# Kernel optimization log

Measured on AMD Instinct MI355X. Metric: run time of the kernel, lower is better.

Reference implementation:

```python
import jax, jax.numpy as jnp
import numpy as np

N = 10000          # nodes
E = 160000         # edges (before self-loops)
F_IN = 256
H, C = 8, 64       # heads, channels per head
NUM_CLASSES = 40
NEG_SLOPE = 0.2    # PyG GATConv default leaky_relu slope


def setup_inputs() -> dict:
    key = jax.random.key(0)
    ks = jax.random.split(key, 16)
    s = 0.1  # keep logits tame
    x = jax.random.normal(ks[0], (N, F_IN), jnp.float32)
    edge_index = jax.random.randint(ks[1], (2, E), 0, N)
    W0 = jax.random.normal(ks[2], (F_IN, H * C), jnp.float32) / np.sqrt(F_IN)
    a_src0 = jax.random.normal(ks[3], (H, C), jnp.float32) * s
    a_dst0 = jax.random.normal(ks[4], (H, C), jnp.float32) * s
    b0 = jnp.zeros((H * C,), jnp.float32)
    W1 = jax.random.normal(ks[5], (H * C, H * C), jnp.float32) / np.sqrt(H * C)
    a_src1 = jax.random.normal(ks[6], (H, C), jnp.float32) * s
    a_dst1 = jax.random.normal(ks[7], (H, C), jnp.float32) * s
    b1 = jnp.zeros((H * C,), jnp.float32)
    W2 = jax.random.normal(ks[8], (H * C, NUM_CLASSES), jnp.float32) / np.sqrt(H * C)
    a_src2 = jax.random.normal(ks[9], (1, NUM_CLASSES), jnp.float32) * s
    a_dst2 = jax.random.normal(ks[10], (1, NUM_CLASSES), jnp.float32) * s
    b2 = jnp.zeros((NUM_CLASSES,), jnp.float32)
    return dict(x=x, edge_index=edge_index, W0=W0, a_src0=a_src0, a_dst0=a_dst0, b0=b0,
                W1=W1, a_src1=a_src1, a_dst1=a_dst1, b1=b1,
                W2=W2, a_src2=a_src2, a_dst2=a_dst2, b2=b2)


def gat_conv(x, src, dst, W, a_src, a_dst, b, concat):
    """PyG GATConv (eval mode: dropout = identity)."""
    n = x.shape[0]
    h, c = a_src.shape
    hx = (x @ W).reshape(n, h, c)                       # [N,H,C]
    al_s = jnp.sum(hx * a_src, axis=-1)                 # [N,H]
    al_d = jnp.sum(hx * a_dst, axis=-1)                 # [N,H]
    e = jax.nn.leaky_relu(al_s[src] + al_d[dst], NEG_SLOPE)  # [E,H]
    # neighbor softmax over incoming edges of each dst node
    m = jax.ops.segment_max(e, dst, num_segments=n)     # [N,H]
    ex = jnp.exp(e - m[dst])
    denom = jax.ops.segment_sum(ex, dst, num_segments=n)
    alpha = ex / (denom[dst] + 1e-16)                   # [E,H]
    msg = hx[src] * alpha[:, :, None]                   # [E,H,C]
    out = jax.ops.segment_sum(msg, dst, num_segments=n) # [N,H,C]
    out = out.reshape(n, h * c) if concat else out.mean(axis=1)
    return out + b


def reference(x, edge_index, W0, a_src0, a_dst0, b0, W1, a_src1, a_dst1, b1,
              W2, a_src2, a_dst2, b2):
    # add self-loops once (PyG GATConv add_self_loops=True)
    loops = jnp.arange(N, dtype=edge_index.dtype)
    src = jnp.concatenate([edge_index[0], loops])
    dst = jnp.concatenate([edge_index[1], loops])
    x = jax.nn.elu(gat_conv(x, src, dst, W0, a_src0, a_dst0, b0, True))
    x = jax.nn.elu(gat_conv(x, src, dst, W1, a_src1, a_dst1, b1, True))
    return gat_conv(x, src, dst, W2, a_src2, a_dst2, b2, False)
```

## Files before the change

### kernel.cpp

```cpp
#include <hip/hip_runtime.h>
#include <math.h>

#define NN 10000
#define EE 160000
#define ET 170000
#define FIN 256
#define HH 8
#define CC 64
#define HC 512
#define NCLS 40
#define ELLW 96

typedef unsigned short u16;
typedef unsigned int u32;
typedef _Float16 f16;
using f16x8 = __attribute__((ext_vector_type(8))) _Float16;
using f32x4 = __attribute__((ext_vector_type(4))) float;

#define MFMA16(a, b, c) __builtin_amdgcn_mfma_f32_16x16x32_f16((a), (b), (c), 0, 0, 0)

__global__ __launch_bounds__(256) void zero_int(int* p, int n) {
    int i = blockIdx.x * 256 + threadIdx.x;
    if (i < n) p[i] = 0;
}

__global__ __launch_bounds__(256) void scatter_ell(const int* __restrict__ ei,
                                                   int* __restrict__ cnt,
                                                   int* __restrict__ ell) {
    int e = blockIdx.x * 256 + threadIdx.x;
    if (e >= ET) return;
    int s, d;
    if (e < EE) { s = ei[e]; d = ei[EE + e]; }
    else        { s = e - EE; d = s; }
    int pos = atomicAdd(&cnt[d], 1);
    if (pos < ELLW) ell[(size_t)d * ELLW + pos] = s;
}

__global__ __launch_bounds__(256) void convW_kernel(const float* __restrict__ W0,
                                                    const float* __restrict__ W1,
                                                    const float* __restrict__ W2,
                                                    f16* __restrict__ w0T,
                                                    f16* __restrict__ w1T,
                                                    f16* __restrict__ w2T) {
    int i = blockIdx.x * 256 + threadIdx.x;
    if (i < HC * FIN) {
        int n = i >> 8, k = i & 255;
        w0T[i] = (f16)W0[(size_t)k * HC + n];
    } else if (i < HC * FIN + HC * HC) {
        int j = i - HC * FIN;
        int n = j >> 9, k = j & 511;
        w1T[j] = (f16)W1[(size_t)k * HC + n];
    } else if (i < HC * FIN + HC * HC + NCLS * HC) {
        int j = i - HC * FIN - HC * HC;
        int n = j >> 9, k = j & 511;
        w2T[j] = (f16)W2[(size_t)k * NCLS + n];
    }
}

template <int K, bool AF32>
__global__ __launch_bounds__(512) void gemm_attn(const void* __restrict__ Aptr,
                                                 const f16* __restrict__ BT,
                                                 const float* __restrict__ a_src,
                                                 const float* __restrict__ a_dst,
                                                 f16* __restrict__ hx2,
                                                 float* __restrict__ al_s,
                                                 float* __restrict__ al_d) {
    constexpr int KK = K / 32;
    constexpr int CH = K / 8;
    __shared__ f16 Bs[64 * K];
    int t = threadIdx.x;
    int hp = blockIdx.x;
    int lane = t & 63, w = t >> 6;
    int fm = lane & 15, g = lane >> 4;
    int bm = blockIdx.y * 128 + w * 16;
    int row = bm + fm;
    bool rok = row < NN;

    f16x8 af[KK];
    if (AF32) {
        const float* A = (const float*)Aptr;
#pragma unroll
        for (int kk = 0; kk < KK; ++kk) {
            float4 lo = make_float4(0.f, 0.f, 0.f, 0.f), hi = lo;
            if (rok) {
                const float* ap = A + (size_t)row * K + kk * 32 + g * 8;
                lo = *(const float4*)ap;
                hi = *(const float4*)(ap + 4);
            }
            f16x8 v;
            v[0] = (f16)lo.x; v[1] = (f16)lo.y; v[2] = (f16)lo.z; v[3] = (f16)lo.w;
            v[4] = (f16)hi.x; v[5] = (f16)hi.y; v[6] = (f16)hi.z; v[7] = (f16)hi.w;
            af[kk] = v;
        }
    } else {
        const f16* A = (const f16*)Aptr;
#pragma unroll
        for (int kk = 0; kk < KK; ++kk) {
            uint4 r = rok ? *(const uint4*)(A + (size_t)row * K + kk * 32 + g * 8)
                          : make_uint4(0u, 0u, 0u, 0u);
            af[kk] = __builtin_bit_cast(f16x8, r);
        }
    }

    for (int sl = 0; sl < 2; ++sl) {
        int h = hp * 2 + sl;
        const f16* bsrc = BT + (size_t)h * 64 * K;
        for (int c = t; c < 64 * CH; c += 512) {
            int brow = c / CH;
            int j = c - brow * CH;
            uint4 v = *(const uint4*)(bsrc + (size_t)brow * K + j * 8);
            *(uint4*)&Bs[(size_t)brow * K + ((j ^ (brow & 7)) * 8)] = v;
        }
        __syncthreads();

        f32x4 acc[4] = {};
#pragma unroll
        for (int kk = 0; kk < KK; ++kk) {
#pragma unroll
            for (int nt = 0; nt < 4; ++nt) {
                f16x8 b = *(const f16x8*)
                    &Bs[(nt * 16 + fm) * K + (((kk * 4 + g) ^ (fm & 7)) * 8)];
                acc[nt] = MFMA16(af[kk], b, acc[nt]);
            }
        }

        float asc[4], adc[4];
#pragma unroll
        for (int nt = 0; nt < 4; ++nt) {
            asc[nt] = a_src[h * 64 + nt * 16 + fm];
            adc[nt] = a_dst[h * 64 + nt * 16 + fm];
        }
#pragma unroll
        for (int r = 0; r < 4; ++r) {
            int orow = bm + g * 4 + r;
            float s = acc[0][r] * asc[0] + acc[1][r] * asc[1] +
                      acc[2][r] * asc[2] + acc[3][r] * asc[3];
            float d = acc[0][r] * adc[0] + acc[1][r] * adc[1] +
                      acc[2][r] * adc[2] + acc[3][r] * adc[3];
#pragma unroll
            for (int off = 1; off < 16; off <<= 1) {
                s += __shfl_xor(s, off);
                d += __shfl_xor(d, off);
            }
            if (orow < NN) {
                if (fm == 0) {
                    al_s[orow * 8 + h] = s;
                    al_d[orow * 8 + h] = d;
                }
#pragma unroll
                for (int nt = 0; nt < 4; ++nt)
                    hx2[(size_t)orow * HC + h * 64 + nt * 16 + fm] =
                        (f16)acc[nt][r];
            }
        }
        __syncthreads();
    }
}

__global__ __launch_bounds__(256) void gemm2_attn(const f16* __restrict__ A,
                                                  const f16* __restrict__ BT,
                                                  const float* __restrict__ a_src2,
                                                  const float* __restrict__ a_dst2,
                                                  float* __restrict__ hx40,
                                                  float* __restrict__ als2,
                                                  float* __restrict__ ald2) {
    __shared__ f16 Bs[48 * HC];
    int t = threadIdx.x;
    int lane = t & 63, w = t >> 6;
    int fm = lane & 15, g = lane >> 4;
    int bm = blockIdx.x * 64 + w * 16;
    int row = bm + fm;
    bool rok = row < NN;

    for (int c = t; c < 48 * 64; c += 256) {
        int brow = c >> 6, j = c & 63;
        uint4 v = make_uint4(0u, 0u, 0u, 0u);
        if (brow < NCLS) v = *(const uint4*)(BT + (size_t)brow * HC + j * 8);
        *(uint4*)&Bs[brow * HC + ((j ^ (brow & 7)) * 8)] = v;
    }

    f16x8 af[16];
#pragma unroll
    for (int kk = 0; kk < 16; ++kk) {
        uint4 r = rok ? *(const uint4*)(A + (size_t)row * HC + kk * 32 + g * 8)
                      : make_uint4(0u, 0u, 0u, 0u);
        af[kk] = __builtin_bit_cast(f16x8, r);
    }
    __syncthreads();

    f32x4 acc[3] = {};
#pragma unroll
    for (int kk = 0; kk < 16; ++kk) {
#pragma unroll
        for (int nt = 0; nt < 3; ++nt) {
            f16x8 b = *(const f16x8*)
                &Bs[(nt * 16 + fm) * HC + (((kk * 4 + g) ^ (fm & 7)) * 8)];
            acc[nt] = MFMA16(af[kk], b, acc[nt]);
        }
    }

    float a2s[3], a2d[3];
#pragma unroll
    for (int nt = 0; nt < 3; ++nt) {
        int col = nt * 16 + fm;
        a2s[nt] = (col < NCLS) ? a_src2[col] : 0.f;
        a2d[nt] = (col < NCLS) ? a_dst2[col] : 0.f;
    }
#pragma unroll
    for (int r = 0; r < 4; ++r) {
        int orow = bm + g * 4 + r;
        float s = acc[0][r] * a2s[0] + acc[1][r] * a2s[1] + acc[2][r] * a2s[2];
        float d = acc[0][r] * a2d[0] + acc[1][r] * a2d[1] + acc[2][r] * a2d[2];
#pragma unroll
        for (int off = 1; off < 16; off <<= 1) {
            s += __shfl_xor(s, off);
            d += __shfl_xor(d, off);
        }
        if (orow < NN) {
            if (fm == 0) { als2[orow] = s; ald2[orow] = d; }
#pragma unroll
            for (int nt = 0; nt < 3; ++nt) {
                int col = nt * 16 + fm;
                if (col < NCLS) hx40[(size_t)orow * NCLS + col] = acc[nt][r];
            }
        }
    }
}

__global__ __launch_bounds__(256) void agg_ell(const f16* __restrict__ hx2,
                                               const float* __restrict__ al_s,
                                               const float* __restrict__ al_d,
                                               const int* __restrict__ cnt,
                                               const int* __restrict__ ell,
                                               const float* __restrict__ bias,
                                               f16* __restrict__ outF) {
    int lane = threadIdx.x & 63, w = threadIdx.x >> 6;
    int n = blockIdx.x * 4 + w;
    if (n >= NN) return;
    int ch = lane * 8;
    int h = lane >> 3;
    float ald = al_d[n * HH + h];
    int dg = cnt[n]; if (dg > ELLW) dg = ELLW;
    const int* ep = ell + (size_t)n * ELLW;
    float acc[8] = {0.f, 0.f, 0.f, 0.f, 0.f, 0.f, 0.f, 0.f};
    float den = 0.f;
    int i = 0;
    for (; i + 4 <= dg; i += 4) {
        int s0 = ep[i], s1 = ep[i + 1], s2 = ep[i + 2], s3 = ep[i + 3];
        float e0 = al_s[s0 * HH + h], e1 = al_s[s1 * HH + h];
        float e2 = al_s[s2 * HH + h], e3 = al_s[s3 * HH + h];
        uint4 v0 = *(const uint4*)(hx2 + (size_t)s0 * HC + ch);
        uint4 v1 = *(const uint4*)(hx2 + (size_t)s1 * HC + ch);
        uint4 v2 = *(const uint4*)(hx2 + (size_t)s2 * HC + ch);
        uint4 v3 = *(const uint4*)(hx2 + (size_t)s3 * HC + ch);
        e0 += ald; e0 = e0 > 0.f ? e0 : 0.2f * e0;
        e1 += ald; e1 = e1 > 0.f ? e1 : 0.2f * e1;
        e2 += ald; e2 = e2 > 0.f ? e2 : 0.2f * e2;
        e3 += ald; e3 = e3 > 0.f ? e3 : 0.2f * e3;
        float w0 = __expf(e0), w1 = __expf(e1), w2 = __expf(e2), w3 = __expf(e3);
        f16x8 f0 = __builtin_bit_cast(f16x8, v0);
        f16x8 f1 = __builtin_bit_cast(f16x8, v1);
        f16x8 f2 = __builtin_bit_cast(f16x8, v2);
        f16x8 f3 = __builtin_bit_cast(f16x8, v3);
#pragma unroll
        for (int j = 0; j < 8; ++j)
            acc[j] += w0 * (float)f0[j] + w1 * (float)f1[j] +
                      w2 * (float)f2[j] + w3 * (float)f3[j];
        den += w0 + w1 + w2 + w3;
    }
    for (; i < dg; ++i) {
        int s = ep[i];
        float e = al_s[s * HH + h] + ald;
        e = e > 0.f ? e : 0.2f * e;
        float wgt = __expf(e);
        uint4 v = *(const uint4*)(hx2 + (size_t)s * HC + ch);
        f16x8 f = __builtin_bit_cast(f16x8, v);
#pragma unroll
        for (int j = 0; j < 8; ++j) acc[j] += wgt * (float)f[j];
        den += wgt;
    }
    float inv = 1.f / (den + 1e-16f);
    float4 b0v = *(const float4*)(bias + ch);
    float4 b1v = *(const float4*)(bias + ch + 4);
    float bb[8] = {b0v.x, b0v.y, b0v.z, b0v.w, b1v.x, b1v.y, b1v.z, b1v.w};
    f16x8 o;
#pragma unroll
    for (int j = 0; j < 8; ++j) {
        float v = acc[j] * inv + bb[j];
        v = v > 0.f ? v : expm1f(v);
        o[j] = (f16)v;
    }
    *(uint4*)(outF + (size_t)n * HC + ch) = __builtin_bit_cast(uint4, o);
}

__global__ __launch_bounds__(64) void agg2_final(const float* __restrict__ hx40,
                                                 const float* __restrict__ als,
                                                 const float* __restrict__ aldp,
                                                 const int* __restrict__ cnt,
                                                 const int* __restrict__ ell,
                                                 const float* __restrict__ b2,
                                                 float* __restrict__ out) {
    int n = blockIdx.x;
    int c = threadIdx.x;
    float ald = aldp[n];
    int dg = cnt[n]; if (dg > ELLW) dg = ELLW;
    const int* ep = ell + (size_t)n * ELLW;
    float acc = 0.f, den = 0.f;
    int i = 0;
    for (; i + 4 <= dg; i += 4) {
        int s0 = ep[i], s1 = ep[i + 1], s2 = ep[i + 2], s3 = ep[i + 3];
        float e0 = als[s0], e1 = als[s1], e2 = als[s2], e3 = als[s3];
        float v0 = 0.f, v1 = 0.f, v2 = 0.f, v3 = 0.f;
        if (c < NCLS) {
            v0 = hx40[(size_t)s0 * NCLS + c];
            v1 = hx40[(size_t)s1 * NCLS + c];
            v2 = hx40[(size_t)s2 * NCLS + c];
            v3 = hx40[(size_t)s3 * NCLS + c];
        }
        e0 += ald; e0 = e0 > 0.f ? e0 : 0.2f * e0;
        e1 += ald; e1 = e1 > 0.f ? e1 : 0.2f * e1;
        e2 += ald; e2 = e2 > 0.f ? e2 : 0.2f * e2;
        e3 += ald; e3 = e3 > 0.f ? e3 : 0.2f * e3;
        float w0 = __expf(e0), w1 = __expf(e1), w2 = __expf(e2), w3 = __expf(e3);
        acc += w0 * v0 + w1 * v1 + w2 * v2 + w3 * v3;
        den += w0 + w1 + w2 + w3;
    }
    for (; i < dg; ++i) {
        int s = ep[i];
        float e = als[s] + ald;
        e = e > 0.f ? e : 0.2f * e;
        float wgt = __expf(e);
        if (c < NCLS) acc += wgt * hx40[(size_t)s * NCLS + c];
        den += wgt;
    }
    if (c < NCLS) out[(size_t)n * NCLS + c] = acc / (den + 1e-16f) + b2[c];
}

extern "C" void kernel_launch(void* const* d_in, const int* in_sizes, int n_in,
                              void* d_out, int out_size, void* d_ws, size_t ws_size,
                              hipStream_t stream) {
    const float* x   = (const float*)d_in[0];
    const int*   ei  = (const int*)  d_in[1];
    const float* W0  = (const float*)d_in[2];
    const float* as0 = (const float*)d_in[3];
    const float* ad0 = (const float*)d_in[4];
    const float* b0  = (const float*)d_in[5];
    const float* W1  = (const float*)d_in[6];
    const float* as1 = (const float*)d_in[7];
    const float* ad1 = (const float*)d_in[8];
    const float* b1  = (const float*)d_in[9];
    const float* W2  = (const float*)d_in[10];
    const float* as2 = (const float*)d_in[11];
    const float* ad2 = (const float*)d_in[12];
    const float* b2  = (const float*)d_in[13];
    float* out = (float*)d_out;

    char* p = (char*)d_ws;
    int* cnt  = (int*)p; p += 40064;
    int* ell  = (int*)p; p += (size_t)NN * ELLW * 4;
    f16* w0T  = (f16*)p; p += HC * FIN * 2;
    f16* w1T  = (f16*)p; p += HC * HC * 2;
    f16* w2T  = (f16*)p; p += NCLS * HC * 2;
    f16* hxA  = (f16*)p; p += (size_t)NN * HC * 2;
    f16* hxB  = (f16*)p; p += (size_t)NN * HC * 2;
    f16* fA   = (f16*)p; p += (size_t)NN * HC * 2;
    f16* fB   = (f16*)p; p += (size_t)NN * HC * 2;
    float* hx40 = (float*)p; p += (size_t)NN * NCLS * 4;
    float* als0 = (float*)p; p += NN * HH * 4;
    float* ald0 = (float*)p; p += NN * HH * 4;
    float* als1 = (float*)p; p += NN * HH * 4;
    float* ald1 = (float*)p; p += NN * HH * 4;
    float* als2 = (float*)p; p += NN * 4;
    float* ald2 = (float*)p; p += NN * 4;

    const int NBR = (NN + 127) / 128;
    const int NAG = (NN + 3) / 4;
    const int NB2 = (NN + 63) / 64;

    zero_int<<<(NN + 255) / 256, 256, 0, stream>>>(cnt, NN);
    scatter_ell<<<(ET + 255) / 256, 256, 0, stream>>>(ei, cnt, ell);
    convW_kernel<<<(HC * FIN + HC * HC + NCLS * HC + 255) / 256, 256, 0, stream>>>(
        W0, W1, W2, w0T, w1T, w2T);

    dim3 gA(4, NBR);
    gemm_attn<FIN, true><<<gA, 512, 0, stream>>>(x, w0T, as0, ad0, hxA, als0, ald0);
    agg_ell<<<NAG, 256, 0, stream>>>(hxA, als0, ald0, cnt, ell, b0, fA);
    gemm_attn<HC, false><<<gA, 512, 0, stream>>>(fA, w1T, as1, ad1, hxB, als1, ald1);
    agg_ell<<<NAG, 256, 0, stream>>>(hxB, als1, ald1, cnt, ell, b1, fB);
    gemm2_attn<<<NB2, 256, 0, stream>>>(fB, w2T, as2, ad2, hx40, als2, ald2);
    agg2_final<<<NN, 64, 0, stream>>>(hx40, als2, ald2, cnt, ell, b2, out);
}
```

Before: 207.5 us.

## Split each node's neighbor aggregation across two waves and fold zeroing into weight conversion

agg_ell now gives each destination node two wavefronts that take alternating neighbors, then combines their partial sums and denominators through shared memory. This doubles the wave count and halves the serial neighbor loop per wave, so more gather loads are in flight. The cost is a block barrier plus LDS traffic. Separately, zeroing the degree counters moves into the weight-conversion kernel, which removes one kernel launch.

```diff
diff --git a/kernel.cpp b/kernel.cpp
--- a/kernel.cpp
+++ b/kernel.cpp
@@ -19,30 +19,15 @@
 
 #define MFMA16(a, b, c) __builtin_amdgcn_mfma_f32_16x16x32_f16((a), (b), (c), 0, 0, 0)
 
-__global__ __launch_bounds__(256) void zero_int(int* p, int n) {
-    int i = blockIdx.x * 256 + threadIdx.x;
-    if (i < n) p[i] = 0;
-}
-
-__global__ __launch_bounds__(256) void scatter_ell(const int* __restrict__ ei,
-                                                   int* __restrict__ cnt,
-                                                   int* __restrict__ ell) {
-    int e = blockIdx.x * 256 + threadIdx.x;
-    if (e >= ET) return;
-    int s, d;
-    if (e < EE) { s = ei[e]; d = ei[EE + e]; }
-    else        { s = e - EE; d = s; }
-    int pos = atomicAdd(&cnt[d], 1);
-    if (pos < ELLW) ell[(size_t)d * ELLW + pos] = s;
-}
-
 __global__ __launch_bounds__(256) void convW_kernel(const float* __restrict__ W0,
                                                     const float* __restrict__ W1,
                                                     const float* __restrict__ W2,
                                                     f16* __restrict__ w0T,
                                                     f16* __restrict__ w1T,
-                                                    f16* __restrict__ w2T) {
+                                                    f16* __restrict__ w2T,
+                                                    int* __restrict__ cnt) {
     int i = blockIdx.x * 256 + threadIdx.x;
+    if (i < NN) cnt[i] = 0;
     if (i < HC * FIN) {
         int n = i >> 8, k = i & 255;
         w0T[i] = (f16)W0[(size_t)k * HC + n];
@@ -55,6 +40,18 @@
         int n = j >> 9, k = j & 511;
         w2T[j] = (f16)W2[(size_t)k * NCLS + n];
     }
+}
+
+__global__ __launch_bounds__(256) void scatter_ell(const int* __restrict__ ei,
+                                                   int* __restrict__ cnt,
+                                                   int* __restrict__ ell) {
+    int e = blockIdx.x * 256 + threadIdx.x;
+    if (e >= ET) return;
+    int s, d;
+    if (e < EE) { s = ei[e]; d = ei[EE + e]; }
+    else        { s = e - EE; d = s; }
+    int pos = atomicAdd(&cnt[d], 1);
+    if (pos < ELLW) ell[(size_t)d * ELLW + pos] = s;
 }
 
 template <int K, bool AF32>
@@ -234,63 +231,81 @@
                                                const int* __restrict__ ell,
                                                const float* __restrict__ bias,
                                                f16* __restrict__ outF) {
-    int lane = threadIdx.x & 63, w = threadIdx.x >> 6;
-    int n = blockIdx.x * 4 + w;
-    if (n >= NN) return;
+    __shared__ float accbuf[2][64][8];
+    __shared__ float denbuf[2][64];
+    int t = threadIdx.x;
+    int lane = t & 63, w = t >> 6;
+    int p = w >> 1, sub = w & 1;
+    int n = blockIdx.x * 2 + p;
+    bool nok = n < NN;
     int ch = lane * 8;
     int h = lane >> 3;
-    float ald = al_d[n * HH + h];
-    int dg = cnt[n]; if (dg > ELLW) dg = ELLW;
-    const int* ep = ell + (size_t)n * ELLW;
     float acc[8] = {0.f, 0.f, 0.f, 0.f, 0.f, 0.f, 0.f, 0.f};
     float den = 0.f;
-    int i = 0;
-    for (; i + 4 <= dg; i += 4) {
-        int s0 = ep[i], s1 = ep[i + 1], s2 = ep[i + 2], s3 = ep[i + 3];
-        float e0 = al_s[s0 * HH + h], e1 = al_s[s1 * HH + h];
-        float e2 = al_s[s2 * HH + h], e3 = al_s[s3 * HH + h];
-        uint4 v0 = *(const uint4*)(hx2 + (size_t)s0 * HC + ch);
-        uint4 v1 = *(const uint4*)(hx2 + (size_t)s1 * HC + ch);
-        uint4 v2 = *(const uint4*)(hx2 + (size_t)s2 * HC + ch);
-        uint4 v3 = *(const uint4*)(hx2 + (size_t)s3 * HC + ch);
-        e0 += ald; e0 = e0 > 0.f ? e0 : 0.2f * e0;
-        e1 += ald; e1 = e1 > 0.f ? e1 : 0.2f * e1;
-        e2 += ald; e2 = e2 > 0.f ? e2 : 0.2f * e2;
-        e3 += ald; e3 = e3 > 0.f ? e3 : 0.2f * e3;
-        float w0 = __expf(e0), w1 = __expf(e1), w2 = __expf(e2), w3 = __expf(e3);
-        f16x8 f0 = __builtin_bit_cast(f16x8, v0);
-        f16x8 f1 = __builtin_bit_cast(f16x8, v1);
-        f16x8 f2 = __builtin_bit_cast(f16x8, v2);
-        f16x8 f3 = __builtin_bit_cast(f16x8, v3);
-#pragma unroll
-        for (int j = 0; j < 8; ++j)
-            acc[j] += w0 * (float)f0[j] + w1 * (float)f1[j] +
-                      w2 * (float)f2[j] + w3 * (float)f3[j];
-        den += w0 + w1 + w2 + w3;
-    }
-    for (; i < dg; ++i) {
-        int s = ep[i];
-        float e = al_s[s * HH + h] + ald;
-        e = e > 0.f ? e : 0.2f * e;
-        float wgt = __expf(e);
-        uint4 v = *(const uint4*)(hx2 + (size_t)s * HC + ch);
-        f16x8 f = __builtin_bit_cast(f16x8, v);
-#pragma unroll
-        for (int j = 0; j < 8; ++j) acc[j] += wgt * (float)f[j];
-        den += wgt;
-    }
-    float inv = 1.f / (den + 1e-16f);
-    float4 b0v = *(const float4*)(bias + ch);
-    float4 b1v = *(const float4*)(bias + ch + 4);
-    float bb[8] = {b0v.x, b0v.y, b0v.z, b0v.w, b1v.x, b1v.y, b1v.z, b1v.w};
-    f16x8 o;
-#pragma unroll
-    for (int j = 0; j < 8; ++j) {
-        float v = acc[j] * inv + bb[j];
-        v = v > 0.f ? v : expm1f(v);
-        o[j] = (f16)v;
-    }
-    *(uint4*)(outF + (size_t)n * HC + ch) = __builtin_bit_cast(uint4, o);
+    if (nok) {
+        float ald = al_d[n * HH + h];
+        int dg = cnt[n]; if (dg > ELLW) dg = ELLW;
+        const int* ep = ell + (size_t)n * ELLW;
+        int i = sub;
+        for (; i + 6 < dg; i += 8) {
+            int s0 = ep[i], s1 = ep[i + 2], s2 = ep[i + 4], s3 = ep[i + 6];
+            float e0 = al_s[s0 * HH + h], e1 = al_s[s1 * HH + h];
+            float e2 = al_s[s2 * HH + h], e3 = al_s[s3 * HH + h];
+            uint4 v0 = *(const uint4*)(hx2 + (size_t)s0 * HC + ch);
+            uint4 v1 = *(const uint4*)(hx2 + (size_t)s1 * HC + ch);
+            uint4 v2 = *(const uint4*)(hx2 + (size_t)s2 * HC + ch);
+            uint4 v3 = *(const uint4*)(hx2 + (size_t)s3 * HC + ch);
+            e0 += ald; e0 = e0 > 0.f ? e0 : 0.2f * e0;
+            e1 += ald; e1 = e1 > 0.f ? e1 : 0.2f * e1;
+            e2 += ald; e2 = e2 > 0.f ? e2 : 0.2f * e2;
+            e3 += ald; e3 = e3 > 0.f ? e3 : 0.2f * e3;
+            float w0 = __expf(e0), w1 = __expf(e1);
+            float w2 = __expf(e2), w3 = __expf(e3);
+            f16x8 f0 = __builtin_bit_cast(f16x8, v0);
+            f16x8 f1 = __builtin_bit_cast(f16x8, v1);
+            f16x8 f2 = __builtin_bit_cast(f16x8, v2);
+            f16x8 f3 = __builtin_bit_cast(f16x8, v3);
+#pragma unroll
+            for (int j = 0; j < 8; ++j)
+                acc[j] += w0 * (float)f0[j] + w1 * (float)f1[j] +
+                          w2 * (float)f2[j] + w3 * (float)f3[j];
+            den += w0 + w1 + w2 + w3;
+        }
+        for (; i < dg; i += 2) {
+            int s = ep[i];
+            float e = al_s[s * HH + h] + ald;
+            e = e > 0.f ? e : 0.2f * e;
+            float wgt = __expf(e);
+            uint4 v = *(const uint4*)(hx2 + (size_t)s * HC + ch);
+            f16x8 f = __builtin_bit_cast(f16x8, v);
+#pragma unroll
+            for (int j = 0; j < 8; ++j) acc[j] += wgt * (float)f[j];
+            den += wgt;
+        }
+    }
+    if (sub == 1) {
+#pragma unroll
+        for (int j = 0; j < 8; ++j) accbuf[p][lane][j] = acc[j];
+        denbuf[p][lane] = den;
+    }
+    __syncthreads();
+    if (sub == 0 && nok) {
+#pragma unroll
+        for (int j = 0; j < 8; ++j) acc[j] += accbuf[p][lane][j];
+        den += denbuf[p][lane];
+        float inv = 1.f / (den + 1e-16f);
+        float4 b0v = *(const float4*)(bias + ch);
+        float4 b1v = *(const float4*)(bias + ch + 4);
+        float bb[8] = {b0v.x, b0v.y, b0v.z, b0v.w, b1v.x, b1v.y, b1v.z, b1v.w};
+        f16x8 o;
+#pragma unroll
+        for (int j = 0; j < 8; ++j) {
+            float v = acc[j] * inv + bb[j];
+            v = v > 0.f ? v : expm1f(v);
+            o[j] = (f16)v;
+        }
+        *(uint4*)(outF + (size_t)n * HC + ch) = __builtin_bit_cast(uint4, o);
+    }
 }
 
 __global__ __launch_bounds__(64) void agg2_final(const float* __restrict__ hx40,
@@ -374,13 +389,12 @@
     float* ald2 = (float*)p; p += NN * 4;
 
     const int NBR = (NN + 127) / 128;
-    const int NAG = (NN + 3) / 4;
+    const int NAG = (NN + 1) / 2;
     const int NB2 = (NN + 63) / 64;
 
-    zero_int<<<(NN + 255) / 256, 256, 0, stream>>>(cnt, NN);
+    convW_kernel<<<(HC * FIN + HC * HC + NCLS * HC + 255) / 256, 256, 0, stream>>>(
+        W0, W1, W2, w0T, w1T, w2T, cnt);
     scatter_ell<<<(ET + 255) / 256, 256, 0, stream>>>(ei, cnt, ell);
-    convW_kernel<<<(HC * FIN + HC * HC + NCLS * HC + 255) / 256, 256, 0, stream>>>(
-        W0, W1, W2, w0T, w1T, w2T);
 
     dim3 gA(4, NBR);
     gemm_attn<FIN, true><<<gA, 512, 0, stream>>>(x, w0T, as0, ad0, hxA, als0, ald0);
```

Result: no change. 207.1 us (-0.2%).

## Store projected features in head-pair slabs and split aggregation across slabs

Applied to the files above, without the earlier changes.

The GEMM epilogue now writes hx into four slabs of 128 channels (two heads each) instead of row-major 512-wide rows. Aggregation launches one block per (slab, node-group), and each wave processes four edges in parallel, 16 lanes per edge, then combines the partial sums with cross-lane shuffles. The aim is to keep each slab's gather working set small enough to stay cache-resident and to raise the number of outstanding gathers. The cost is that each edge index and attention logit is read four times, one per slab. Separately, the count zeroing becomes a memset and the scatter and weight-conversion kernels merge into one launch.

```diff
diff --git a/kernel.cpp b/kernel.cpp
--- a/kernel.cpp
+++ b/kernel.cpp
@@ -19,30 +19,28 @@
 
 #define MFMA16(a, b, c) __builtin_amdgcn_mfma_f32_16x16x32_f16((a), (b), (c), 0, 0, 0)
 
-__global__ __launch_bounds__(256) void zero_int(int* p, int n) {
-    int i = blockIdx.x * 256 + threadIdx.x;
-    if (i < n) p[i] = 0;
-}
-
-__global__ __launch_bounds__(256) void scatter_ell(const int* __restrict__ ei,
+#define SCAT_BLOCKS 665
+__global__ __launch_bounds__(256) void prep_kernel(const int* __restrict__ ei,
                                                    int* __restrict__ cnt,
-                                                   int* __restrict__ ell) {
-    int e = blockIdx.x * 256 + threadIdx.x;
-    if (e >= ET) return;
-    int s, d;
-    if (e < EE) { s = ei[e]; d = ei[EE + e]; }
-    else        { s = e - EE; d = s; }
-    int pos = atomicAdd(&cnt[d], 1);
-    if (pos < ELLW) ell[(size_t)d * ELLW + pos] = s;
-}
-
-__global__ __launch_bounds__(256) void convW_kernel(const float* __restrict__ W0,
-                                                    const float* __restrict__ W1,
-                                                    const float* __restrict__ W2,
-                                                    f16* __restrict__ w0T,
-                                                    f16* __restrict__ w1T,
-                                                    f16* __restrict__ w2T) {
-    int i = blockIdx.x * 256 + threadIdx.x;
+                                                   int* __restrict__ ell,
+                                                   const float* __restrict__ W0,
+                                                   const float* __restrict__ W1,
+                                                   const float* __restrict__ W2,
+                                                   f16* __restrict__ w0T,
+                                                   f16* __restrict__ w1T,
+                                                   f16* __restrict__ w2T) {
+    int b = blockIdx.x;
+    if (b < SCAT_BLOCKS) {
+        int e = b * 256 + threadIdx.x;
+        if (e >= ET) return;
+        int s, d;
+        if (e < EE) { s = ei[e]; d = ei[EE + e]; }
+        else        { s = e - EE; d = s; }
+        int pos = atomicAdd(&cnt[d], 1);
+        if (pos < ELLW) ell[(size_t)d * ELLW + pos] = s;
+        return;
+    }
+    int i = (b - SCAT_BLOCKS) * 256 + threadIdx.x;
     if (i < HC * FIN) {
         int n = i >> 8, k = i & 255;
         w0T[i] = (f16)W0[(size_t)k * HC + n];
@@ -130,6 +128,7 @@
             asc[nt] = a_src[h * 64 + nt * 16 + fm];
             adc[nt] = a_dst[h * 64 + nt * 16 + fm];
         }
+        f16* hxslab = hx2 + ((size_t)(h >> 1) * NN) * 128 + (h & 1) * 64;
 #pragma unroll
         for (int r = 0; r < 4; ++r) {
             int orow = bm + g * 4 + r;
@@ -149,8 +148,7 @@
                 }
 #pragma unroll
                 for (int nt = 0; nt < 4; ++nt)
-                    hx2[(size_t)orow * HC + h * 64 + nt * 16 + fm] =
-                        (f16)acc[nt][r];
+                    hxslab[(size_t)orow * 128 + nt * 16 + fm] = (f16)acc[nt][r];
             }
         }
         __syncthreads();
@@ -227,70 +225,62 @@
     }
 }
 
-__global__ __launch_bounds__(256) void agg_ell(const f16* __restrict__ hx2,
-                                               const float* __restrict__ al_s,
-                                               const float* __restrict__ al_d,
-                                               const int* __restrict__ cnt,
-                                               const int* __restrict__ ell,
-                                               const float* __restrict__ bias,
-                                               f16* __restrict__ outF) {
+__global__ __launch_bounds__(256) void agg_slab(const f16* __restrict__ hx2,
+                                                const float* __restrict__ al_s,
+                                                const float* __restrict__ al_d,
+                                                const int* __restrict__ cnt,
+                                                const int* __restrict__ ell,
+                                                const float* __restrict__ bias,
+                                                f16* __restrict__ outF) {
+    int j = blockIdx.x;
+    int slab = j / 2500;
+    int nb = j - slab * 2500;
     int lane = threadIdx.x & 63, w = threadIdx.x >> 6;
-    int n = blockIdx.x * 4 + w;
-    if (n >= NN) return;
-    int ch = lane * 8;
-    int h = lane >> 3;
+    int n = nb * 4 + w;
+    int grp = lane >> 4, li = lane & 15;
+    int h = slab * 2 + (li >> 3);
+    const f16* slabp = hx2 + (size_t)slab * NN * 128;
     float ald = al_d[n * HH + h];
     int dg = cnt[n]; if (dg > ELLW) dg = ELLW;
     const int* ep = ell + (size_t)n * ELLW;
     float acc[8] = {0.f, 0.f, 0.f, 0.f, 0.f, 0.f, 0.f, 0.f};
     float den = 0.f;
-    int i = 0;
-    for (; i + 4 <= dg; i += 4) {
-        int s0 = ep[i], s1 = ep[i + 1], s2 = ep[i + 2], s3 = ep[i + 3];
-        float e0 = al_s[s0 * HH + h], e1 = al_s[s1 * HH + h];
-        float e2 = al_s[s2 * HH + h], e3 = al_s[s3 * HH + h];
-        uint4 v0 = *(const uint4*)(hx2 + (size_t)s0 * HC + ch);
-        uint4 v1 = *(const uint4*)(hx2 + (size_t)s1 * HC + ch);
-        uint4 v2 = *(const uint4*)(hx2 + (size_t)s2 * HC + ch);
-        uint4 v3 = *(const uint4*)(hx2 + (size_t)s3 * HC + ch);
-        e0 += ald; e0 = e0 > 0.f ? e0 : 0.2f * e0;
-        e1 += ald; e1 = e1 > 0.f ? e1 : 0.2f * e1;
-        e2 += ald; e2 = e2 > 0.f ? e2 : 0.2f * e2;
-        e3 += ald; e3 = e3 > 0.f ? e3 : 0.2f * e3;
-        float w0 = __expf(e0), w1 = __expf(e1), w2 = __expf(e2), w3 = __expf(e3);
-        f16x8 f0 = __builtin_bit_cast(f16x8, v0);
-        f16x8 f1 = __builtin_bit_cast(f16x8, v1);
-        f16x8 f2 = __builtin_bit_cast(f16x8, v2);
-        f16x8 f3 = __builtin_bit_cast(f16x8, v3);
-#pragma unroll
-        for (int j = 0; j < 8; ++j)
-            acc[j] += w0 * (float)f0[j] + w1 * (float)f1[j] +
-                      w2 * (float)f2[j] + w3 * (float)f3[j];
-        den += w0 + w1 + w2 + w3;
-    }
-    for (; i < dg; ++i) {
-        int s = ep[i];
+#pragma unroll 2
+    for (int base = 0; base < dg; base += 4) {
+        int i = base + grp;
+        bool valid = i < dg;
+        int s = valid ? ep[i] : 0;
         float e = al_s[s * HH + h] + ald;
         e = e > 0.f ? e : 0.2f * e;
-        float wgt = __expf(e);
-        uint4 v = *(const uint4*)(hx2 + (size_t)s * HC + ch);
-        f16x8 f = __builtin_bit_cast(f16x8, v);
-#pragma unroll
-        for (int j = 0; j < 8; ++j) acc[j] += wgt * (float)f[j];
-        den += wgt;
-    }
-    float inv = 1.f / (den + 1e-16f);
-    float4 b0v = *(const float4*)(bias + ch);
-    float4 b1v = *(const float4*)(bias + ch + 4);
-    float bb[8] = {b0v.x, b0v.y, b0v.z, b0v.w, b1v.x, b1v.y, b1v.z, b1v.w};
-    f16x8 o;
-#pragma unroll
-    for (int j = 0; j < 8; ++j) {
-        float v = acc[j] * inv + bb[j];
-        v = v > 0.f ? v : expm1f(v);
-        o[j] = (f16)v;
-    }
-    *(uint4*)(outF + (size_t)n * HC + ch) = __builtin_bit_cast(uint4, o);
+        float wt = valid ? __expf(e) : 0.f;
+        uint4 raw = *(const uint4*)(slabp + (size_t)s * 128 + li * 8);
+        f16x8 f = __builtin_bit_cast(f16x8, raw);
+#pragma unroll
+        for (int c = 0; c < 8; ++c) acc[c] += wt * (float)f[c];
+        den += wt;
+    }
+    den += __shfl_xor(den, 16);
+    den += __shfl_xor(den, 32);
+#pragma unroll
+    for (int c = 0; c < 8; ++c) {
+        acc[c] += __shfl_xor(acc[c], 16);
+        acc[c] += __shfl_xor(acc[c], 32);
+    }
+    if (grp == 0) {
+        int col = slab * 128 + li * 8;
+        float inv = 1.f / (den + 1e-16f);
+        float4 b0v = *(const float4*)(bias + col);
+        float4 b1v = *(const float4*)(bias + col + 4);
+        float bb[8] = {b0v.x, b0v.y, b0v.z, b0v.w, b1v.x, b1v.y, b1v.z, b1v.w};
+        f16x8 o;
+#pragma unroll
+        for (int c = 0; c < 8; ++c) {
+            float v = acc[c] * inv + bb[c];
+            v = v > 0.f ? v : expm1f(v);
+            o[c] = (f16)v;
+        }
+        *(uint4*)(outF + (size_t)n * HC + col) = __builtin_bit_cast(uint4, o);
+    }
 }
 
 __global__ __launch_bounds__(64) void agg2_final(const float* __restrict__ hx40,
@@ -374,19 +364,17 @@
     float* ald2 = (float*)p; p += NN * 4;
 
     const int NBR = (NN + 127) / 128;
-    const int NAG = (NN + 3) / 4;
     const int NB2 = (NN + 63) / 64;
-
-    zero_int<<<(NN + 255) / 256, 256, 0, stream>>>(cnt, NN);
-    scatter_ell<<<(ET + 255) / 256, 256, 0, stream>>>(ei, cnt, ell);
-    convW_kernel<<<(HC * FIN + HC * HC + NCLS * HC + 255) / 256, 256, 0, stream>>>(
-        W0, W1, W2, w0T, w1T, w2T);
+    const int NPREP = SCAT_BLOCKS + (HC * FIN + HC * HC + NCLS * HC + 255) / 256;
+
+    hipMemsetAsync(cnt, 0, NN * sizeof(int), stream);
+    prep_kernel<<<NPREP, 256, 0, stream>>>(ei, cnt, ell, W0, W1, W2, w0T, w1T, w2T);
 
     dim3 gA(4, NBR);
     gemm_attn<FIN, true><<<gA, 512, 0, stream>>>(x, w0T, as0, ad0, hxA, als0, ald0);
-    agg_ell<<<NAG, 256, 0, stream>>>(hxA, als0, ald0, cnt, ell, b0, fA);
+    agg_slab<<<10000, 256, 0, stream>>>(hxA, als0, ald0, cnt, ell, b0, fA);
     gemm_attn<HC, false><<<gA, 512, 0, stream>>>(fA, w1T, as1, ad1, hxB, als1, ald1);
-    agg_ell<<<NAG, 256, 0, stream>>>(hxB, als1, ald1, cnt, ell, b1, fB);
+    agg_slab<<<10000, 256, 0, stream>>>(hxB, als1, ald1, cnt, ell, b1, fB);
     gemm2_attn<<<NB2, 256, 0, stream>>>(fB, w2T, as2, ad2, hx40, als2, ald2);
     agg2_final<<<NN, 64, 0, stream>>>(hx40, als2, ald2, cnt, ell, b2, out);
 }
```

New measurement: 228.0 us. 1.1x slower.
